# Optimization experiments

Measured on AMD Instinct MI355X. Metric: run time of the kernel, lower is better.

## Reference

```python
import jax, jax.numpy as jnp
import numpy as np

N_NODES = 100000
N_EDGES = 1600000
DIM = 128
N_BUNDLES = 8
BUNDLE_DIM = 4
HIDDEN = 256
TIME = 2


def setup_inputs() -> dict:
    key = jax.random.key(0)
    ks = jax.random.split(key, 8)
    x = jax.random.normal(ks[0], (N_NODES, DIM), dtype=jnp.float32)
    node_rep = jax.random.normal(ks[1], (N_NODES, N_BUNDLES, BUNDLE_DIM, BUNDLE_DIM), dtype=jnp.float32)
    # edge list; ensure every node has out-degree >= 1 so degree norm is finite
    src_extra = jax.random.randint(ks[2], (N_EDGES - N_NODES,), 0, N_NODES)
    src = jnp.concatenate([jnp.arange(N_NODES), src_extra]).astype(jnp.int64)
    dst = jax.random.randint(ks[3], (N_EDGES,), 0, N_NODES).astype(jnp.int64)
    w1 = jax.random.normal(ks[4], (HIDDEN, DIM), dtype=jnp.float32) * (1.0 / np.sqrt(DIM))
    b1 = jnp.zeros((HIDDEN,), dtype=jnp.float32)
    w2 = jax.random.normal(ks[5], (DIM, HIDDEN), dtype=jnp.float32) * (1.0 / np.sqrt(HIDDEN))
    b2 = jnp.zeros((DIM,), dtype=jnp.float32)
    return {"x": x, "node_rep": node_rep, "src": src, "dst": dst,
            "w1": w1, "b1": b1, "w2": w2, "b2": b2}


def reference(x, node_rep, src, dst, w1, b1, w2, b2):
    n = x.shape[0]
    # out-degrees (number of edges with node as source)
    deg = jax.ops.segment_sum(jnp.ones_like(src, dtype=x.dtype), src, num_segments=n)
    # u_mul_v: per-edge product of src and dst degrees -> symmetric norm coefs
    norm_coefs = jax.lax.rsqrt(deg[src] * deg[dst])  # [E]
    # per-bundle rotation: einsum('abcd,abde->abce', node_rep, vf)
    vf = x.reshape(n, N_BUNDLES, BUNDLE_DIM, -1)
    vf = jnp.einsum('nbcd,nbde->nbce', node_rep, vf)
    h = vf.reshape(n, DIM)
    # u_mul_e_sum repeated `time` times: out[dst] += h[src] * coef
    for _ in range(TIME):
        h = jax.ops.segment_sum(h[src] * norm_coefs[:, None], dst, num_segments=n)
    # inverse rotation with transposed node_rep
    vf = h.reshape(n, N_BUNDLES, BUNDLE_DIM, -1)
    vf = jnp.einsum('nbdc,nbde->nbce', node_rep, vf)
    h = vf.reshape(n, DIM)
    # feed-forward (dropout=0, exact GELU as in torch nn.GELU default)
    h = jax.nn.gelu(h @ w1.T + b1, approximate=False)
    return h @ w2.T + b2
```

## Files before the change

kernel.cpp:

```cpp
#include <hip/hip_runtime.h>
#include <hip/hip_bf16.h>
#include <math.h>

#define DIM 128
#define HID 256

typedef short s8x __attribute__((ext_vector_type(8)));
typedef float f4x __attribute__((ext_vector_type(4)));

__device__ __forceinline__ unsigned short f2bf(float f) {
    unsigned int u = __float_as_uint(f);
    u += 0x7FFF + ((u >> 16) & 1);
    return (unsigned short)(u >> 16);
}
__device__ __forceinline__ float bf2f(unsigned short b) {
    return __uint_as_float(((unsigned int)b) << 16);
}
__device__ __forceinline__ float bflo(unsigned int p) {
    return __uint_as_float(p << 16);
}
__device__ __forceinline__ float bfhi(unsigned int p) {
    return __uint_as_float(p & 0xffff0000u);
}


__global__ __launch_bounds__(256) void hist_kernel(
        const int* __restrict__ src, const int* __restrict__ dst,
        int* __restrict__ TD, int* __restrict__ TS, int nE, int nbuck, int chunk,
        int NBE) {
    __shared__ int hd[1024], hs[1024];
    const int tid = threadIdx.x, blk = blockIdx.x;
    for (int b = tid; b < nbuck; b += 256) { hd[b] = 0; hs[b] = 0; }
    __syncthreads();
    int beg = blk * chunk, end = min(beg + chunk, nE);
    for (int i = beg + tid; i < end; i += 256) {
        atomicAdd(&hd[dst[i] >> 7], 1);
        atomicAdd(&hs[src[i] >> 7], 1);
    }
    __syncthreads();
    for (int b = tid; b < nbuck; b += 256) {
        TD[b * NBE + blk] = hd[b];
        TS[b * NBE + blk] = hs[b];
    }
}

__global__ void scan_blocks(const int* in, int* out, int* bsums, int n) {
    __shared__ int part[256];
    const int tid = threadIdx.x;
    const int base = blockIdx.x * 1024 + tid * 4;
    int v[4];
    int sum = 0;
#pragma unroll
    for (int k = 0; k < 4; ++k) {
        v[k] = (base + k < n) ? in[base + k] : 0;
        sum += v[k];
    }
    part[tid] = sum;
    __syncthreads();
    for (int off = 1; off < 256; off <<= 1) {
        int t = (tid >= off) ? part[tid - off] : 0;
        __syncthreads();
        part[tid] += t;
        __syncthreads();
    }
    int excl = part[tid] - sum;
    if (tid == 255) bsums[blockIdx.x] = part[255];
#pragma unroll
    for (int k = 0; k < 4; ++k) {
        if (base + k < n) out[base + k] = excl;
        excl += v[k];
    }
}

__global__ void scan_sums(int* bsums, int nb) {
    __shared__ int part[256];
    const int tid = threadIdx.x;
    const int base = tid * 8;
    int v[8];
    int sum = 0;
#pragma unroll
    for (int k = 0; k < 8; ++k) {
        v[k] = (base + k < nb) ? bsums[base + k] : 0;
        sum += v[k];
    }
    part[tid] = sum;
    __syncthreads();
    for (int off = 1; off < 256; off <<= 1) {
        int t = (tid >= off) ? part[tid - off] : 0;
        __syncthreads();
        part[tid] += t;
        __syncthreads();
    }
    int excl = part[tid] - sum;
#pragma unroll
    for (int k = 0; k < 8; ++k) {
        if (base + k < nb) bsums[base + k] = excl;
        excl += v[k];
    }
}

__global__ void scan_add(int* T, const int* __restrict__ bsums, int n2, int half, int E) {
    int i = blockIdx.x * blockDim.x + threadIdx.x;
    if (i < n2) {
        int v = T[i] + bsums[i >> 10];
        T[i] = (i >= half) ? v - E : v;
    }
}

__global__ __launch_bounds__(256) void scatter_edges(
        const int* __restrict__ src, const int* __restrict__ dst,
        const int* __restrict__ TD, const int* __restrict__ TS,
        unsigned int* __restrict__ pairs, unsigned char* __restrict__ sbyte,
        int nE, int nbuck, int chunk, int NBE) {
    __shared__ int cd[1024], cs[1024];
    const int tid = threadIdx.x, blk = blockIdx.x;
    for (int b = tid; b < nbuck; b += 256) {
        cd[b] = TD[b * NBE + blk];
        cs[b] = TS[b * NBE + blk];
    }
    __syncthreads();
    int beg = blk * chunk, end = min(beg + chunk, nE);
    for (int i = beg + tid; i < end; i += 256) {
        int s = src[i], d = dst[i];
        int pd = atomicAdd(&cd[d >> 7], 1);
        pairs[pd] = ((unsigned)s << 7) | (unsigned)(d & 127);
        int ps = atomicAdd(&cs[s >> 7], 1);
        sbyte[ps] = (unsigned char)(s & 127);
    }
}

__global__ __launch_bounds__(256) void finalize_src(
        const unsigned char* __restrict__ sbyte, const int* __restrict__ TS,
        float* __restrict__ rdeg, int nE, int nbuck, int nN, int NBE) {
    __shared__ int hist[128];
    const int tid = threadIdx.x, b = blockIdx.x;
    if (tid < 128) hist[tid] = 0;
    __syncthreads();
    int beg = TS[b * NBE];
    int end = (b + 1 < nbuck) ? TS[(b + 1) * NBE] : nE;
    for (int i = beg + tid; i < end; i += 256)
        atomicAdd(&hist[sbyte[i]], 1);
    __syncthreads();
    if (tid < 128) {
        int idx = (b << 7) + tid;
        if (idx < nN) rdeg[idx] = rsqrtf((float)hist[tid]);
    }
}

template<bool PACK>
__global__ __launch_bounds__(256) void finalize_dst(
        const unsigned int* __restrict__ pairs, const int* __restrict__ TD,
        const float* __restrict__ rdeg,
        int* __restrict__ rowstart, uint2* __restrict__ ecsr,
        int* __restrict__ esrcA, int nE, int nbuck, int nN, int NBE) {
    __shared__ int hist[128], sbuf[128], cur[128];
    const int tid = threadIdx.x, b = blockIdx.x;
    int beg = TD[b * NBE];
    int end = (b + 1 < nbuck) ? TD[(b + 1) * NBE] : nE;
    if (tid < 128) hist[tid] = 0;
    __syncthreads();
    for (int i = beg + tid; i < end; i += 256)
        atomicAdd(&hist[(int)(pairs[i] & 127u)], 1);
    __syncthreads();
    int v = (tid < 128) ? hist[tid] : 0;
    if (tid < 128) sbuf[tid] = v;
    __syncthreads();
    for (int off = 1; off < 128; off <<= 1) {
        int t = (tid < 128 && tid >= off) ? sbuf[tid - off] : 0;
        __syncthreads();
        if (tid < 128) sbuf[tid] += t;
        __syncthreads();
    }
    if (tid < 128) {
        int excl = sbuf[tid] - v;
        cur[tid] = excl;
        int idx = (b << 7) + tid;
        if (idx <= nN) rowstart[idx] = beg + excl;
    }
    __syncthreads();
    for (int i = beg + tid; i < end; i += 256) {
        unsigned int p = pairs[i];
        int l = (int)(p & 127u);
        int s = (int)(p >> 7);
        int pos = atomicAdd(&cur[l], 1);
        if (PACK) {
            float coef = rdeg[s] * rdeg[(b << 7) + l];
            ecsr[beg + pos] = make_uint2((unsigned)s, __float_as_uint(coef));
        } else {
            esrcA[beg + pos] = s;
        }
    }
}

__global__ void rot_cvt_kernel(const float* __restrict__ x, const float* __restrict__ R,
                               unsigned short* __restrict__ h0,
                               const float* __restrict__ w1, const float* __restrict__ w2,
                               unsigned short* __restrict__ w1b, unsigned short* __restrict__ w2b,
                               int n, int nbRot) {
    if ((int)blockIdx.x >= nbRot) {
        int t = (blockIdx.x - nbRot) * 256 + threadIdx.x;
        for (int i = t; i < 32768; i += 4096) {
            w1b[i] = f2bf(w1[i]);
            w2b[i] = f2bf(w2[i]);
        }
        return;
    }
    int u = blockIdx.x * blockDim.x + threadIdx.x;
    if (u >= n * 8) return;
    int nd = u >> 3, b = u & 7;
    const float* xp = &x[(size_t)nd * DIM + b * 16];
    const float* Rp = &R[(size_t)nd * DIM + b * 16];
    float xv[16], rv[16];
#pragma unroll
    for (int d = 0; d < 4; ++d) {
        *(float4*)&xv[d * 4] = *(const float4*)&xp[d * 4];
        *(float4*)&rv[d * 4] = *(const float4*)&Rp[d * 4];
    }
    unsigned short ob[16];
#pragma unroll
    for (int c = 0; c < 4; ++c)
#pragma unroll
        for (int e = 0; e < 4; ++e) {
            float acc = 0.f;
#pragma unroll
            for (int d = 0; d < 4; ++d) acc += rv[c * 4 + d] * xv[d * 4 + e];
            ob[c * 4 + e] = f2bf(acc);
        }
    unsigned short* op = &h0[(size_t)nd * DIM + b * 16];
    *(s8x*)&op[0] = *(s8x*)&ob[0];
    *(s8x*)&op[8] = *(s8x*)&ob[8];
}

template<bool PACK>
__global__ __launch_bounds__(256) void gather_kernel(
        const unsigned short* __restrict__ hsrc,
        const uint2* __restrict__ ecsr, const int* __restrict__ esrcA,
        const float* __restrict__ rdeg, const int* __restrict__ rowstart,
        unsigned short* __restrict__ hdst, int n) {
    const int node = blockIdx.x * 16 + (threadIdx.x >> 4);
    const int lane = threadIdx.x & 15;
    if (node >= n) return;
    const int beg = rowstart[node];
    const int end = rowstart[node + 1];
    float rd = 0.f;
    if (!PACK) rd = rdeg[node];
    float a0 = 0.f, a1 = 0.f, a2 = 0.f, a3 = 0.f;
    float a4 = 0.f, a5 = 0.f, a6 = 0.f, a7 = 0.f;
    int i = beg;
    for (; i + 4 <= end; i += 4) {
        int s0, s1, s2, s3;
        float c0, c1, c2, c3;
        if (PACK) {
            uint2 e0 = ecsr[i], e1 = ecsr[i + 1], e2 = ecsr[i + 2], e3 = ecsr[i + 3];
            s0 = (int)e0.x; c0 = __uint_as_float(e0.y);
            s1 = (int)e1.x; c1 = __uint_as_float(e1.y);
            s2 = (int)e2.x; c2 = __uint_as_float(e2.y);
            s3 = (int)e3.x; c3 = __uint_as_float(e3.y);
        } else {
            s0 = esrcA[i]; s1 = esrcA[i + 1]; s2 = esrcA[i + 2]; s3 = esrcA[i + 3];
            c0 = rdeg[s0] * rd; c1 = rdeg[s1] * rd;
            c2 = rdeg[s2] * rd; c3 = rdeg[s3] * rd;
        }
        uint4 p0 = *(const uint4*)&hsrc[(size_t)s0 * DIM + lane * 8];
        uint4 p1 = *(const uint4*)&hsrc[(size_t)s1 * DIM + lane * 8];
        uint4 p2 = *(const uint4*)&hsrc[(size_t)s2 * DIM + lane * 8];
        uint4 p3 = *(const uint4*)&hsrc[(size_t)s3 * DIM + lane * 8];
        a0 += bflo(p0.x) * c0 + bflo(p1.x) * c1 + bflo(p2.x) * c2 + bflo(p3.x) * c3;
        a1 += bfhi(p0.x) * c0 + bfhi(p1.x) * c1 + bfhi(p2.x) * c2 + bfhi(p3.x) * c3;
        a2 += bflo(p0.y) * c0 + bflo(p1.y) * c1 + bflo(p2.y) * c2 + bflo(p3.y) * c3;
        a3 += bfhi(p0.y) * c0 + bfhi(p1.y) * c1 + bfhi(p2.y) * c2 + bfhi(p3.y) * c3;
        a4 += bflo(p0.z) * c0 + bflo(p1.z) * c1 + bflo(p2.z) * c2 + bflo(p3.z) * c3;
        a5 += bfhi(p0.z) * c0 + bfhi(p1.z) * c1 + bfhi(p2.z) * c2 + bfhi(p3.z) * c3;
        a6 += bflo(p0.w) * c0 + bflo(p1.w) * c1 + bflo(p2.w) * c2 + bflo(p3.w) * c3;
        a7 += bfhi(p0.w) * c0 + bfhi(p1.w) * c1 + bfhi(p2.w) * c2 + bfhi(p3.w) * c3;
    }
    for (; i < end; ++i) {
        int s0;
        float c0;
        if (PACK) {
            uint2 e0 = ecsr[i];
            s0 = (int)e0.x; c0 = __uint_as_float(e0.y);
        } else {
            s0 = esrcA[i];
            c0 = rdeg[s0] * rd;
        }
        uint4 p0 = *(const uint4*)&hsrc[(size_t)s0 * DIM + lane * 8];
        a0 += bflo(p0.x) * c0;
        a1 += bfhi(p0.x) * c0;
        a2 += bflo(p0.y) * c0;
        a3 += bfhi(p0.y) * c0;
        a4 += bflo(p0.z) * c0;
        a5 += bfhi(p0.z) * c0;
        a6 += bflo(p0.w) * c0;
        a7 += bfhi(p0.w) * c0;
    }
    uint4 o;
    o.x = (unsigned)f2bf(a0) | ((unsigned)f2bf(a1) << 16);
    o.y = (unsigned)f2bf(a2) | ((unsigned)f2bf(a3) << 16);
    o.z = (unsigned)f2bf(a4) | ((unsigned)f2bf(a5) << 16);
    o.w = (unsigned)f2bf(a6) | ((unsigned)f2bf(a7) << 16);
    *(uint4*)&hdst[(size_t)node * DIM + lane * 8] = o;
}

#define ABST 136
#define HBST 264
__global__ __launch_bounds__(256, 6) void ffn_kernel(
        const unsigned short* __restrict__ h,
        const float* __restrict__ R,
        const unsigned short* __restrict__ w1b,
        const float* __restrict__ b1,
        const unsigned short* __restrict__ w2b,
        const float* __restrict__ b2,
        float* __restrict__ out, int n) {
    __shared__ unsigned short smem[32 * HBST];
    unsigned short* abuf = smem;
    unsigned short* hbuf = smem;
    const int tid  = threadIdx.x;
    const int node0 = blockIdx.x * 32;
    const int wave = tid >> 6;
    const int lane = tid & 63;
    const int lr = lane & 15;
    const int lq = lane >> 4;

    {
        int nd = tid >> 3, b = tid & 7;
        int gn = node0 + nd;
        float hv[16], rv[16];
        if (gn < n) {
            const unsigned short* hp = &h[(size_t)gn * DIM + b * 16];
            const float* Rp = &R[(size_t)gn * DIM + b * 16];
            unsigned short hraw[16];
            *(s8x*)&hraw[0] = *(const s8x*)&hp[0];
            *(s8x*)&hraw[8] = *(const s8x*)&hp[8];
#pragma unroll
            for (int d = 0; d < 16; ++d) hv[d] = bf2f(hraw[d]);
#pragma unroll
            for (int d = 0; d < 4; ++d)
                *(float4*)&rv[d * 4] = *(const float4*)&Rp[d * 4];
        } else {
#pragma unroll
            for (int d = 0; d < 16; ++d) { hv[d] = 0.f; rv[d] = 0.f; }
        }
#pragma unroll
        for (int c = 0; c < 4; ++c) {
            unsigned short gb[4];
#pragma unroll
            for (int e = 0; e < 4; ++e) {
                float acc = 0.f;
#pragma unroll
                for (int d = 0; d < 4; ++d) acc += rv[d * 4 + c] * hv[d * 4 + e];
                gb[e] = f2bf(acc);
            }
            *(ushort4*)&abuf[nd * ABST + b * 16 + c * 4] =
                make_ushort4(gb[0], gb[1], gb[2], gb[3]);
        }
    }
    __syncthreads();

    f4x acc1[2][4];
#pragma unroll
    for (int mt = 0; mt < 2; ++mt)
#pragma unroll
        for (int nt = 0; nt < 4; ++nt) acc1[mt][nt] = (f4x){0.f, 0.f, 0.f, 0.f};

    const int nw = wave * 64;
    for (int ks = 0; ks < 4; ++ks) {
        const int k0 = ks * 32 + lq * 8;
        s8x af[2], bfv[4];
#pragma unroll
        for (int mt = 0; mt < 2; ++mt)
            af[mt] = *(const s8x*)&abuf[(mt * 16 + lr) * ABST + k0];
#pragma unroll
        for (int nt = 0; nt < 4; ++nt)
            bfv[nt] = *(const s8x*)&w1b[(size_t)(nw + nt * 16 + lr) * 128 + k0];
#pragma unroll
        for (int mt = 0; mt < 2; ++mt)
#pragma unroll
            for (int nt = 0; nt < 4; ++nt)
                acc1[mt][nt] = __builtin_amdgcn_mfma_f32_16x16x32_bf16(
                    af[mt], bfv[nt], acc1[mt][nt], 0, 0, 0);
    }
    __syncthreads();

#pragma unroll
    for (int nt = 0; nt < 4; ++nt) {
        int nn = nw + nt * 16 + lr;
        float bias = b1[nn];
#pragma unroll
        for (int mt = 0; mt < 2; ++mt) {
#pragma unroll
            for (int r = 0; r < 4; ++r) {
                float v = acc1[mt][nt][r] + bias;
                v = 0.5f * v * (1.f + erff(v * 0.70710678118654752f));
                hbuf[(mt * 16 + lq * 4 + r) * HBST + nn] = f2bf(v);
            }
        }
    }
    __syncthreads();

    f4x acc2[2][2];
#pragma unroll
    for (int mt = 0; mt < 2; ++mt)
#pragma unroll
        for (int nt = 0; nt < 2; ++nt) acc2[mt][nt] = (f4x){0.f, 0.f, 0.f, 0.f};

    const int nw2 = wave * 32;
    for (int ks = 0; ks < 8; ++ks) {
        const int k0 = ks * 32 + lq * 8;
        s8x af[2], bf2v[2];
#pragma unroll
        for (int mt = 0; mt < 2; ++mt)
            af[mt] = *(const s8x*)&hbuf[(mt * 16 + lr) * HBST + k0];
#pragma unroll
        for (int nt = 0; nt < 2; ++nt)
            bf2v[nt] = *(const s8x*)&w2b[(size_t)(nw2 + nt * 16 + lr) * 256 + k0];
#pragma unroll
        for (int mt = 0; mt < 2; ++mt)
#pragma unroll
            for (int nt = 0; nt < 2; ++nt)
                acc2[mt][nt] = __builtin_amdgcn_mfma_f32_16x16x32_bf16(
                    af[mt], bf2v[nt], acc2[mt][nt], 0, 0, 0);
    }
#pragma unroll
    for (int nt = 0; nt < 2; ++nt) {
        int n2 = nw2 + nt * 16 + lr;
        float bias = b2[n2];
#pragma unroll
        for (int mt = 0; mt < 2; ++mt) {
#pragma unroll
            for (int r = 0; r < 4; ++r) {
                int gn = node0 + mt * 16 + lq * 4 + r;
                if (gn < n) out[(size_t)gn * DIM + n2] = acc2[mt][nt][r] + bias;
            }
        }
    }
}

extern "C" void kernel_launch(void* const* d_in, const int* in_sizes, int n_in,
                              void* d_out, int out_size, void* d_ws, size_t ws_size,
                              hipStream_t stream) {
    const float* x   = (const float*)d_in[0];
    const float* R   = (const float*)d_in[1];
    const int*   src = (const int*)d_in[2];
    const int*   dst = (const int*)d_in[3];
    const float* w1  = (const float*)d_in[4];
    const float* b1  = (const float*)d_in[5];
    const float* w2  = (const float*)d_in[6];
    const float* b2  = (const float*)d_in[7];
    float* out = (float*)d_out;

    const int N = in_sizes[0] / DIM;
    const int E = in_sizes[2];

    const int nbuck = (N + 127) >> 7;

    const size_t fixed_bytes = (size_t)N * DIM * 4;
    auto tail_bytes = [&](int nbe) {
        return (size_t)N * 4 + (size_t)(N + 1) * 4 +
               (size_t)nbuck * nbe * 8 + 2048 * 4 + (size_t)2 * 32768 * 2;
    };
    int NBE = 1024;
    bool use_pack = true;
    if (fixed_bytes + (size_t)E * 8 + tail_bytes(1024) > ws_size) {
        if (fixed_bytes + (size_t)E * 8 + tail_bytes(256) <= ws_size) {
            NBE = 256;
        } else {
            NBE = 256;
            use_pack = false;
        }
    }
    const int chunk = (E + NBE - 1) / NBE;
    const int nScan = nbuck * NBE;
    const int nScan2 = 2 * nScan;
    const int nbScan2 = (nScan2 + 1023) / 1024;

    unsigned short* hA = (unsigned short*)d_ws;
    unsigned short* hM = hA + (size_t)N * DIM;
    unsigned int*  pairs = (unsigned int*)hM;
    unsigned char* sbyte = (unsigned char*)(pairs + E);
    char* edge_base = (char*)(hM + (size_t)N * DIM);
    const size_t edge_bytes = use_pack ? (size_t)E * 8 : (size_t)E * 4;

    uint2* ecsr  = (uint2*)edge_base;
    int*   esrcA = (int*)edge_base;
    char* q = edge_base + edge_bytes;
    float* rdeg     = (float*)q;
    int*   rowstart = (int*)(rdeg + N);
    int*   TD       = rowstart + (N + 1);
    int*   TS       = TD + nScan;
    int*   bsums    = TS + nScan;
    unsigned short* w1b = (unsigned short*)(bsums + 2048);
    unsigned short* w2b = w1b + 32768;

    const int BLK = 256;

    hist_kernel<<<NBE, BLK, 0, stream>>>(src, dst, TD, TS, E, nbuck, chunk, NBE);
    scan_blocks<<<nbScan2, BLK, 0, stream>>>(TD, TD, bsums, nScan2);
    scan_sums<<<1, BLK, 0, stream>>>(bsums, nbScan2);
    scan_add<<<(nScan2 + BLK - 1) / BLK, BLK, 0, stream>>>(TD, bsums, nScan2, nScan, E);
    scatter_edges<<<NBE, BLK, 0, stream>>>(src, dst, TD, TS, pairs, sbyte, E, nbuck, chunk, NBE);
    finalize_src<<<nbuck, BLK, 0, stream>>>(sbyte, TS, rdeg, E, nbuck, N, NBE);
    if (use_pack)
        finalize_dst<true><<<nbuck, BLK, 0, stream>>>(pairs, TD, rdeg, rowstart,
                                                      ecsr, esrcA, E, nbuck, N, NBE);
    else
        finalize_dst<false><<<nbuck, BLK, 0, stream>>>(pairs, TD, rdeg, rowstart,
                                                       ecsr, esrcA, E, nbuck, N, NBE);

    const int nbRot = ((size_t)N * 8 + BLK - 1) / BLK;
    rot_cvt_kernel<<<nbRot + 16, BLK, 0, stream>>>(x, R, hA, w1, w2, w1b, w2b, N, nbRot);

    const int nbG = (N + 15) / 16;
    if (use_pack) {
        gather_kernel<true><<<nbG, BLK, 0, stream>>>(hA, ecsr, esrcA, rdeg,
                                                     rowstart, hM, N);
        gather_kernel<true><<<nbG, BLK, 0, stream>>>(hM, ecsr, esrcA, rdeg,
                                                     rowstart, hA, N);
    } else {
        gather_kernel<false><<<nbG, BLK, 0, stream>>>(hA, ecsr, esrcA, rdeg,
                                                      rowstart, hM, N);
        gather_kernel<false><<<nbG, BLK, 0, stream>>>(hM, ecsr, esrcA, rdeg,
                                                      rowstart, hA, N);
    }

    ffn_kernel<<<(N + 31) / 32, BLK, 0, stream>>>(hA, R, w1b, b1, w2b, b2, out, N);
}
```

Baseline: 444.1 us.

## Make FFN kernel persistent with next-tile prefetch and fix edge bucket count

```diff
diff --git a/kernel.cpp b/kernel.cpp
--- a/kernel.cpp
+++ b/kernel.cpp
@@ -304,135 +304,174 @@
 
 #define ABST 136
 #define HBST 264
-__global__ __launch_bounds__(256, 6) void ffn_kernel(
+__global__ __launch_bounds__(256, 4) void ffn_kernel(
         const unsigned short* __restrict__ h,
         const float* __restrict__ R,
         const unsigned short* __restrict__ w1b,
         const float* __restrict__ b1,
         const unsigned short* __restrict__ w2b,
         const float* __restrict__ b2,
-        float* __restrict__ out, int n) {
+        float* __restrict__ out, int n, int ntiles) {
     __shared__ unsigned short smem[32 * HBST];
     unsigned short* abuf = smem;
     unsigned short* hbuf = smem;
     const int tid  = threadIdx.x;
-    const int node0 = blockIdx.x * 32;
     const int wave = tid >> 6;
     const int lane = tid & 63;
     const int lr = lane & 15;
     const int lq = lane >> 4;
-
-    {
-        int nd = tid >> 3, b = tid & 7;
-        int gn = node0 + nd;
-        float hv[16], rv[16];
+    const int nd = tid >> 3;
+    const int b  = tid & 7;
+
+    int tile = blockIdx.x;
+
+    s8x hc0 = {0,0,0,0,0,0,0,0}, hc1 = {0,0,0,0,0,0,0,0};
+    float4 rc0 = make_float4(0.f,0.f,0.f,0.f);
+    float4 rc1 = rc0, rc2 = rc0, rc3 = rc0;
+    if (tile < ntiles) {
+        const int gn = tile * 32 + nd;
         if (gn < n) {
             const unsigned short* hp = &h[(size_t)gn * DIM + b * 16];
+            hc0 = *(const s8x*)&hp[0];
+            hc1 = *(const s8x*)&hp[8];
             const float* Rp = &R[(size_t)gn * DIM + b * 16];
-            unsigned short hraw[16];
-            *(s8x*)&hraw[0] = *(const s8x*)&hp[0];
-            *(s8x*)&hraw[8] = *(const s8x*)&hp[8];
-#pragma unroll
-            for (int d = 0; d < 16; ++d) hv[d] = bf2f(hraw[d]);
-#pragma unroll
-            for (int d = 0; d < 4; ++d)
-                *(float4*)&rv[d * 4] = *(const float4*)&Rp[d * 4];
-        } else {
-#pragma unroll
-            for (int d = 0; d < 16; ++d) { hv[d] = 0.f; rv[d] = 0.f; }
-        }
-#pragma unroll
-        for (int c = 0; c < 4; ++c) {
-            unsigned short gb[4];
-#pragma unroll
-            for (int e = 0; e < 4; ++e) {
-                float acc = 0.f;
-#pragma unroll
-                for (int d = 0; d < 4; ++d) acc += rv[d * 4 + c] * hv[d * 4 + e];
-                gb[e] = f2bf(acc);
+            rc0 = *(const float4*)&Rp[0];
+            rc1 = *(const float4*)&Rp[4];
+            rc2 = *(const float4*)&Rp[8];
+            rc3 = *(const float4*)&Rp[12];
+        }
+    }
+
+    while (tile < ntiles) {
+        const int node0 = tile * 32;
+
+        {
+            float hv[16], rv[16];
+#pragma unroll
+            for (int d = 0; d < 8; ++d) {
+                hv[d]     = bf2f((unsigned short)hc0[d]);
+                hv[d + 8] = bf2f((unsigned short)hc1[d]);
             }
-            *(ushort4*)&abuf[nd * ABST + b * 16 + c * 4] =
-                make_ushort4(gb[0], gb[1], gb[2], gb[3]);
-        }
-    }
-    __syncthreads();
-
-    f4x acc1[2][4];
-#pragma unroll
-    for (int mt = 0; mt < 2; ++mt)
-#pragma unroll
-        for (int nt = 0; nt < 4; ++nt) acc1[mt][nt] = (f4x){0.f, 0.f, 0.f, 0.f};
-
-    const int nw = wave * 64;
-    for (int ks = 0; ks < 4; ++ks) {
-        const int k0 = ks * 32 + lq * 8;
-        s8x af[2], bfv[4];
+            *(float4*)&rv[0]  = rc0;
+            *(float4*)&rv[4]  = rc1;
+            *(float4*)&rv[8]  = rc2;
+            *(float4*)&rv[12] = rc3;
+#pragma unroll
+            for (int c = 0; c < 4; ++c) {
+                unsigned short gb[4];
+#pragma unroll
+                for (int e = 0; e < 4; ++e) {
+                    float acc = 0.f;
+#pragma unroll
+                    for (int d = 0; d < 4; ++d) acc += rv[d * 4 + c] * hv[d * 4 + e];
+                    gb[e] = f2bf(acc);
+                }
+                *(ushort4*)&abuf[nd * ABST + b * 16 + c * 4] =
+                    make_ushort4(gb[0], gb[1], gb[2], gb[3]);
+            }
+        }
+        __syncthreads();
+
+        const int tile2 = tile + gridDim.x;
+        s8x hn0 = {0,0,0,0,0,0,0,0}, hn1 = {0,0,0,0,0,0,0,0};
+        float4 rn0 = make_float4(0.f,0.f,0.f,0.f);
+        float4 rn1 = rn0, rn2 = rn0, rn3 = rn0;
+        if (tile2 < ntiles) {
+            const int gn2 = tile2 * 32 + nd;
+            if (gn2 < n) {
+                const unsigned short* hp = &h[(size_t)gn2 * DIM + b * 16];
+                hn0 = *(const s8x*)&hp[0];
+                hn1 = *(const s8x*)&hp[8];
+                const float* Rp = &R[(size_t)gn2 * DIM + b * 16];
+                rn0 = *(const float4*)&Rp[0];
+                rn1 = *(const float4*)&Rp[4];
+                rn2 = *(const float4*)&Rp[8];
+                rn3 = *(const float4*)&Rp[12];
+            }
+        }
+
+        f4x acc1[2][4];
 #pragma unroll
         for (int mt = 0; mt < 2; ++mt)
-            af[mt] = *(const s8x*)&abuf[(mt * 16 + lr) * ABST + k0];
-#pragma unroll
-        for (int nt = 0; nt < 4; ++nt)
-            bfv[nt] = *(const s8x*)&w1b[(size_t)(nw + nt * 16 + lr) * 128 + k0];
+#pragma unroll
+            for (int nt = 0; nt < 4; ++nt) acc1[mt][nt] = (f4x){0.f, 0.f, 0.f, 0.f};
+
+        const int nw = wave * 64;
+        for (int ks = 0; ks < 4; ++ks) {
+            const int k0 = ks * 32 + lq * 8;
+            s8x af[2], bfv[4];
+#pragma unroll
+            for (int mt = 0; mt < 2; ++mt)
+                af[mt] = *(const s8x*)&abuf[(mt * 16 + lr) * ABST + k0];
+#pragma unroll
+            for (int nt = 0; nt < 4; ++nt)
+                bfv[nt] = *(const s8x*)&w1b[(size_t)(nw + nt * 16 + lr) * 128 + k0];
+#pragma unroll
+            for (int mt = 0; mt < 2; ++mt)
+#pragma unroll
+                for (int nt = 0; nt < 4; ++nt)
+                    acc1[mt][nt] = __builtin_amdgcn_mfma_f32_16x16x32_bf16(
+                        af[mt], bfv[nt], acc1[mt][nt], 0, 0, 0);
+        }
+        __syncthreads();
+
+#pragma unroll
+        for (int nt = 0; nt < 4; ++nt) {
+            int nn = nw + nt * 16 + lr;
+            float bias = b1[nn];
+#pragma unroll
+            for (int mt = 0; mt < 2; ++mt) {
+#pragma unroll
+                for (int r = 0; r < 4; ++r) {
+                    float v = acc1[mt][nt][r] + bias;
+                    v = 0.5f * v * (1.f + erff(v * 0.70710678118654752f));
+                    hbuf[(mt * 16 + lq * 4 + r) * HBST + nn] = f2bf(v);
+                }
+            }
+        }
+        __syncthreads();
+
+        f4x acc2[2][2];
 #pragma unroll
         for (int mt = 0; mt < 2; ++mt)
 #pragma unroll
-            for (int nt = 0; nt < 4; ++nt)
-                acc1[mt][nt] = __builtin_amdgcn_mfma_f32_16x16x32_bf16(
-                    af[mt], bfv[nt], acc1[mt][nt], 0, 0, 0);
-    }
-    __syncthreads();
-
-#pragma unroll
-    for (int nt = 0; nt < 4; ++nt) {
-        int nn = nw + nt * 16 + lr;
-        float bias = b1[nn];
-#pragma unroll
-        for (int mt = 0; mt < 2; ++mt) {
-#pragma unroll
-            for (int r = 0; r < 4; ++r) {
-                float v = acc1[mt][nt][r] + bias;
-                v = 0.5f * v * (1.f + erff(v * 0.70710678118654752f));
-                hbuf[(mt * 16 + lq * 4 + r) * HBST + nn] = f2bf(v);
+            for (int nt = 0; nt < 2; ++nt) acc2[mt][nt] = (f4x){0.f, 0.f, 0.f, 0.f};
+
+        const int nw2 = wave * 32;
+        for (int ks = 0; ks < 8; ++ks) {
+            const int k0 = ks * 32 + lq * 8;
+            s8x af[2], bf2v[2];
+#pragma unroll
+            for (int mt = 0; mt < 2; ++mt)
+                af[mt] = *(const s8x*)&hbuf[(mt * 16 + lr) * HBST + k0];
+#pragma unroll
+            for (int nt = 0; nt < 2; ++nt)
+                bf2v[nt] = *(const s8x*)&w2b[(size_t)(nw2 + nt * 16 + lr) * 256 + k0];
+#pragma unroll
+            for (int mt = 0; mt < 2; ++mt)
+#pragma unroll
+                for (int nt = 0; nt < 2; ++nt)
+                    acc2[mt][nt] = __builtin_amdgcn_mfma_f32_16x16x32_bf16(
+                        af[mt], bf2v[nt], acc2[mt][nt], 0, 0, 0);
+        }
+#pragma unroll
+        for (int nt = 0; nt < 2; ++nt) {
+            int n2 = nw2 + nt * 16 + lr;
+            float bias = b2[n2];
+#pragma unroll
+            for (int mt = 0; mt < 2; ++mt) {
+#pragma unroll
+                for (int r = 0; r < 4; ++r) {
+                    int gn = node0 + mt * 16 + lq * 4 + r;
+                    if (gn < n) out[(size_t)gn * DIM + n2] = acc2[mt][nt][r] + bias;
+                }
             }
         }
-    }
-    __syncthreads();
-
-    f4x acc2[2][2];
-#pragma unroll
-    for (int mt = 0; mt < 2; ++mt)
-#pragma unroll
-        for (int nt = 0; nt < 2; ++nt) acc2[mt][nt] = (f4x){0.f, 0.f, 0.f, 0.f};
-
-    const int nw2 = wave * 32;
-    for (int ks = 0; ks < 8; ++ks) {
-        const int k0 = ks * 32 + lq * 8;
-        s8x af[2], bf2v[2];
-#pragma unroll
-        for (int mt = 0; mt < 2; ++mt)
-            af[mt] = *(const s8x*)&hbuf[(mt * 16 + lr) * HBST + k0];
-#pragma unroll
-        for (int nt = 0; nt < 2; ++nt)
-            bf2v[nt] = *(const s8x*)&w2b[(size_t)(nw2 + nt * 16 + lr) * 256 + k0];
-#pragma unroll
-        for (int mt = 0; mt < 2; ++mt)
-#pragma unroll
-            for (int nt = 0; nt < 2; ++nt)
-                acc2[mt][nt] = __builtin_amdgcn_mfma_f32_16x16x32_bf16(
-                    af[mt], bf2v[nt], acc2[mt][nt], 0, 0, 0);
-    }
-#pragma unroll
-    for (int nt = 0; nt < 2; ++nt) {
-        int n2 = nw2 + nt * 16 + lr;
-        float bias = b2[n2];
-#pragma unroll
-        for (int mt = 0; mt < 2; ++mt) {
-#pragma unroll
-            for (int r = 0; r < 4; ++r) {
-                int gn = node0 + mt * 16 + lq * 4 + r;
-                if (gn < n) out[(size_t)gn * DIM + n2] = acc2[mt][nt][r] + bias;
-            }
-        }
+        __syncthreads();
+
+        hc0 = hn0; hc1 = hn1;
+        rc0 = rn0; rc1 = rn1; rc2 = rn2; rc3 = rn3;
+        tile = tile2;
     }
 }
 
@@ -453,22 +492,7 @@
     const int E = in_sizes[2];
 
     const int nbuck = (N + 127) >> 7;
-
-    const size_t fixed_bytes = (size_t)N * DIM * 4;
-    auto tail_bytes = [&](int nbe) {
-        return (size_t)N * 4 + (size_t)(N + 1) * 4 +
-               (size_t)nbuck * nbe * 8 + 2048 * 4 + (size_t)2 * 32768 * 2;
-    };
-    int NBE = 1024;
-    bool use_pack = true;
-    if (fixed_bytes + (size_t)E * 8 + tail_bytes(1024) > ws_size) {
-        if (fixed_bytes + (size_t)E * 8 + tail_bytes(256) <= ws_size) {
-            NBE = 256;
-        } else {
-            NBE = 256;
-            use_pack = false;
-        }
-    }
+    const int NBE = 256;
     const int chunk = (E + NBE - 1) / NBE;
     const int nScan = nbuck * NBE;
     const int nScan2 = 2 * nScan;
@@ -479,6 +503,11 @@
     unsigned int*  pairs = (unsigned int*)hM;
     unsigned char* sbyte = (unsigned char*)(pairs + E);
     char* edge_base = (char*)(hM + (size_t)N * DIM);
+
+    const size_t tail_bytes = (size_t)N * 4 + (size_t)(N + 1) * 4 +
+                              (size_t)nScan * 8 + 2048 * 4 + (size_t)2 * 32768 * 2;
+    const size_t fixed_bytes = (size_t)N * DIM * 4;
+    const bool use_pack = (fixed_bytes + (size_t)E * 8 + tail_bytes) <= ws_size;
     const size_t edge_bytes = use_pack ? (size_t)E * 8 : (size_t)E * 4;
 
     uint2* ecsr  = (uint2*)edge_base;
@@ -523,5 +552,7 @@
                                                       rowstart, hA, N);
     }
 
-    ffn_kernel<<<(N + 31) / 32, BLK, 0, stream>>>(hA, R, w1b, b1, w2b, b2, out, N);
-}
+    const int ntiles = (N + 31) / 32;
+    const int nbF = (ntiles < 1024) ? ntiles : 1024;
+    ffn_kernel<<<nbF, BLK, 0, stream>>>(hA, R, w1b, b1, w2b, b2, out, N, ntiles);
+}
```

Result: slower. 463.8 us (+4.4%).
